# Kernel tuning notes

Hardware: AMD Instinct MI355X
Metric: run time of the kernel (lower is better)

## Reference

```python
import jax, jax.numpy as jnp
import numpy as np
from jax import lax

B, HIST, FC, N, F = 64, 24, 24, 1000, 8
EMB, HID, NEMB, OUT = 32, 64, 1000, 1
IN = EMB + OUT  # GRU input dim


def setup_inputs() -> dict:
    key = jax.random.key(0)
    ks = jax.random.split(key, 11)
    X = jax.random.normal(ks[0], (B, HIST + FC, N, F), jnp.float32)
    idx = jax.random.randint(ks[1], (B, HIST + FC, N), 0, NEMB)
    X = X.at[..., -1].set(idx.astype(jnp.float32))  # last channel = spatial ids
    hn = jax.random.normal(ks[2], (B * N, HID), jnp.float32)
    xn = jax.random.normal(ks[3], (B, N, OUT), jnp.float32)
    s = 0.1
    emb_table = jax.random.normal(ks[4], (NEMB, EMB), jnp.float32) * s
    W_ih = jax.random.normal(ks[5], (3 * HID, IN), jnp.float32) * s
    W_hh = jax.random.normal(ks[6], (3 * HID, HID), jnp.float32) * s
    b_ih = jax.random.normal(ks[7], (3 * HID,), jnp.float32) * s
    b_hh = jax.random.normal(ks[8], (3 * HID,), jnp.float32) * s
    W_out = jax.random.normal(ks[9], (OUT, HID), jnp.float32) * s
    b_out = jax.random.normal(ks[10], (OUT,), jnp.float32) * s
    return {"X": X, "hn": hn, "xn": xn, "emb_table": emb_table,
            "W_ih": W_ih, "W_hh": W_hh, "b_ih": b_ih, "b_hh": b_hh,
            "W_out": W_out, "b_out": b_out}


def reference(X, hn, xn, emb_table, W_ih, W_hh, b_ih, b_hh, W_out, b_out):
    # indices for the forecast steps: [FC, B, N]
    idx_seq = X[:, :FC, :, -1].astype(jnp.int32).transpose(1, 0, 2)

    def step(carry, idx_t):
        h, x_prev = carry                      # h: [B*N, HID], x_prev: [B, N, 1]
        emb = emb_table[idx_t]                 # [B, N, EMB] gather
        x = jnp.concatenate([x_prev, emb], axis=-1).reshape(B * N, IN)
        gi = x @ W_ih.T + b_ih                 # [B*N, 3*HID]
        gh = h @ W_hh.T + b_hh
        i_r, i_z, i_n = jnp.split(gi, 3, axis=-1)
        h_r, h_z, h_n = jnp.split(gh, 3, axis=-1)
        r = jax.nn.sigmoid(i_r + h_r)
        z = jax.nn.sigmoid(i_z + h_z)
        n = jnp.tanh(i_n + r * h_n)
        h_new = (1.0 - z) * n + z * h
        out = h_new.reshape(B, N, HID) @ W_out.T + b_out  # [B, N, 1]
        return (h_new, out), out

    _, preds = lax.scan(step, (hn, xn), idx_seq)  # preds: [FC, B, N, 1]
    return preds.transpose(1, 0, 2, 3)            # [B, FC, N, 1]
```

## Files before the change

kernel.cpp:

```cpp
#include <hip/hip_runtime.h>
#include <math.h>

#define BB   64
#define FC   24
#define NN   1000
#define HID  64
#define EMBD 32
#define TT   48
#define FF   8
#define INSZ 33

#define CPB  32
#define TPB  256
#define AST  72
#define XST  40

#define NL2E (-1.4426950408889634f)
#define TL2E ( 2.8853900817779268f)

typedef __attribute__((ext_vector_type(8))) short bf16x8;
typedef __attribute__((ext_vector_type(4))) float f32x4;

static __device__ __forceinline__ unsigned short f2bf(float f) {
    unsigned u = __builtin_bit_cast(unsigned, f);
    u += 0x7FFFu + ((u >> 16) & 1u);
    return (unsigned short)(u >> 16);
}
static __device__ __forceinline__ unsigned cvt_pk_bf16(float a, float b) {
    unsigned r;
    asm("v_cvt_pk_bf16_f32 %0, %1, %2" : "=v"(r) : "v"(a), "v"(b));
    return r;
}
static __device__ __forceinline__ bf16x8 mk_bf8(float4 lo, float4 hi, float s) {
    union { unsigned u[4]; bf16x8 v; } r;
    r.u[0] = cvt_pk_bf16(lo.x * s, lo.y * s);
    r.u[1] = cvt_pk_bf16(lo.z * s, lo.w * s);
    r.u[2] = cvt_pk_bf16(hi.x * s, hi.y * s);
    r.u[3] = cvt_pk_bf16(hi.z * s, hi.w * s);
    return r.v;
}

static __device__ __forceinline__ void lds_barrier() {
    __builtin_amdgcn_sched_barrier(0);
    asm volatile("s_waitcnt lgkmcnt(0)" ::: "memory");
    __builtin_amdgcn_s_barrier();
    __builtin_amdgcn_sched_barrier(0);
}

__global__ __launch_bounds__(TPB) __attribute__((amdgpu_waves_per_eu(3)))
void gru_decoder(
    const float* __restrict__ X,
    const float* __restrict__ hn0,
    const float* __restrict__ xn,
    const float* __restrict__ emb,
    const float* __restrict__ Wih,
    const float* __restrict__ Whh,
    const float* __restrict__ bih,
    const float* __restrict__ bhh,
    const float* __restrict__ Wout,
    const float* __restrict__ bout,
    float* __restrict__ out)
{
    __shared__ __align__(16) unsigned short Abuf[CPB * AST];
    __shared__ __align__(16) unsigned short Xt[2][CPB * XST];
    __shared__ int   idxbuf[FC * CPB];
    __shared__ float xbuf[CPB];

    const int tid  = threadIdx.x;
    const int lane = tid & 63;
    const int g    = tid >> 6;
    const int quad = lane >> 4;
    const int l15  = lane & 15;
    const int jcol = g * 16 + l15;
    const int rowb = quad * 4;
    const int cell0 = blockIdx.x * CPB;

    for (int e = tid; e < FC * CPB; e += TPB) {
        int t = e >> 5, m = e & 31;
        int cell = cell0 + m;
        int b = cell / NN, n = cell - b * NN;
        idxbuf[t * CPB + m] = (int)X[(((size_t)b * TT + t) * NN + n) * FF + 7];
    }
    if (tid < CPB) xbuf[tid] = xn[cell0 + tid];

    bf16x8 Bf[3][2];
    #pragma unroll
    for (int gate = 0; gate < 3; ++gate) {
        const float s = (gate < 2) ? NL2E : TL2E;
        #pragma unroll
        for (int ks = 0; ks < 2; ++ks) {
            const float* src = Whh + (size_t)(gate * HID + jcol) * HID + ks * 32 + quad * 8;
            Bf[gate][ks] = mk_bf8(*(const float4*)src, *(const float4*)(src + 4), s);
        }
    }
    bf16x8 BX[3];
    #pragma unroll
    for (int gate = 0; gate < 3; ++gate) {
        const float s = (gate < 2) ? NL2E : TL2E;
        const float* src = Wih + (size_t)(gate * HID + jcol) * INSZ + 1 + quad * 8;
        union { unsigned u[4]; bf16x8 v; } f;
        #pragma unroll
        for (int p = 0; p < 4; ++p)
            f.u[p] = cvt_pk_bf16(src[2 * p] * s, src[2 * p + 1] * s);
        BX[gate] = f.v;
    }

    const float w0r2 = NL2E * Wih[(size_t)jcol * INSZ];
    const float w0z2 = NL2E * Wih[(size_t)(HID + jcol) * INSZ];
    const float w0n2 = TL2E * Wih[(size_t)(2 * HID + jcol) * INSZ];
    const float br2  = NL2E * (bih[jcol] + bhh[jcol]);
    const float bz2  = NL2E * (bih[HID + jcol] + bhh[HID + jcol]);
    const float bni2 = TL2E * bih[2 * HID + jcol];
    const float bhn2 = TL2E * bhh[2 * HID + jcol];
    const float bout0 = bout[0];

    float wout4[4];
    #pragma unroll
    for (int e2 = 0; e2 < 4; ++e2) wout4[e2] = Wout[l15 * 4 + e2];
    const int od_c = g * 4 + quad;
    size_t ob[2];
    #pragma unroll
    for (int gx = 0; gx < 2; ++gx) {
        int cell = cell0 + gx * 16 + od_c;
        int b = cell / NN, n = cell - b * NN;
        ob[gx] = (size_t)b * FC * NN + n;
    }

    float hold0[4], hold1[4];
    #pragma unroll
    for (int rr = 0; rr < 4; ++rr) {
        int m0 = rowb + rr, m1 = 16 + rowb + rr;
        float h0 = hn0[((size_t)cell0 + m0) * HID + jcol];
        float h1 = hn0[((size_t)cell0 + m1) * HID + jcol];
        hold0[rr] = h0; hold1[rr] = h1;
        Abuf[m0 * AST + jcol] = f2bf(h0);
        Abuf[m1 * AST + jcol] = f2bf(h1);
    }
    __syncthreads();

    const int r8 = tid >> 3, k4 = (tid & 7) * 4;
    {
        int idx = idxbuf[r8];
        float4 e4 = *(const float4*)(emb + (size_t)idx * EMBD + k4);
        *(uint2*)&Xt[0][r8 * XST + k4] =
            make_uint2(cvt_pk_bf16(e4.x, e4.y), cvt_pk_bf16(e4.z, e4.w));
    }
    __syncthreads();

    auto PHASE_A = [&](int X16, const unsigned short* Xc,
                       f32x4& ar, f32x4& az, f32x4& ani, f32x4& ang) {
        const bf16x8 a0 = *(const bf16x8*)&Abuf[(X16 + l15) * AST + quad * 8];
        const bf16x8 a1 = *(const bf16x8*)&Abuf[(X16 + l15) * AST + 32 + quad * 8];
        const bf16x8 x0 = *(const bf16x8*)&Xc[(X16 + l15) * XST + quad * 8];
        const f32x4 z4 = {0.f, 0.f, 0.f, 0.f};
        ar  = __builtin_amdgcn_mfma_f32_16x16x32_bf16(x0, BX[0], z4, 0, 0, 0);
        ar  = __builtin_amdgcn_mfma_f32_16x16x32_bf16(a0, Bf[0][0], ar, 0, 0, 0);
        ar  = __builtin_amdgcn_mfma_f32_16x16x32_bf16(a1, Bf[0][1], ar, 0, 0, 0);
        az  = __builtin_amdgcn_mfma_f32_16x16x32_bf16(x0, BX[1], z4, 0, 0, 0);
        az  = __builtin_amdgcn_mfma_f32_16x16x32_bf16(a0, Bf[1][0], az, 0, 0, 0);
        az  = __builtin_amdgcn_mfma_f32_16x16x32_bf16(a1, Bf[1][1], az, 0, 0, 0);
        ani = __builtin_amdgcn_mfma_f32_16x16x32_bf16(x0, BX[2], z4, 0, 0, 0);
        ang = __builtin_amdgcn_mfma_f32_16x16x32_bf16(a0, Bf[2][0], z4, 0, 0, 0);
        ang = __builtin_amdgcn_mfma_f32_16x16x32_bf16(a1, Bf[2][1], ang, 0, 0, 0);
    };

    auto PHASE_B = [&](int X16, f32x4& ar, f32x4& az, f32x4& ani, f32x4& ang,
                       float* hold) {
        #pragma unroll
        for (int rp = 0; rp < 2; ++rp) {
            float h2[2];
            #pragma unroll
            for (int k = 0; k < 2; ++k) {
                const int rr = rp * 2 + k;
                const int m  = X16 + rowb + rr;
                const float xp = xbuf[m];
                float sr = fmaf(w0r2, xp, ar[rr] + br2);
                float r  = __builtin_amdgcn_rcpf(1.0f + __builtin_amdgcn_exp2f(sr));
                float sz = fmaf(w0z2, xp, az[rr] + bz2);
                float z  = __builtin_amdgcn_rcpf(1.0f + __builtin_amdgcn_exp2f(sz));
                float v  = fmaf(r, ang[rr] + bhn2, fmaf(w0n2, xp, ani[rr] + bni2));
                float e  = __builtin_amdgcn_exp2f(v);
                float nv = fmaf(-2.0f, __builtin_amdgcn_rcpf(e + 1.0f), 1.0f);
                float hnew = fmaf(z, hold[rr] - nv, nv);
                hold[rr] = hnew;
                h2[k] = hnew;
            }
            unsigned pk = cvt_pk_bf16(h2[0], h2[1]);
            const int m0 = X16 + rowb + rp * 2;
            Abuf[m0 * AST + jcol]       = (unsigned short)pk;
            Abuf[(m0 + 1) * AST + jcol] = (unsigned short)(pk >> 16);
        }
    };

    auto OUTDOT = [&](int gx, int tw, bool wr) {
        const int X16 = gx << 4;
        const uint2 hv = *(const uint2*)&Abuf[(X16 + od_c) * AST + l15 * 4];
        float o;
        o = wout4[0] * __builtin_bit_cast(float, hv.x << 16);
        o = fmaf(wout4[1], __builtin_bit_cast(float, hv.x & 0xFFFF0000u), o);
        o = fmaf(wout4[2], __builtin_bit_cast(float, hv.y << 16), o);
        o = fmaf(wout4[3], __builtin_bit_cast(float, hv.y & 0xFFFF0000u), o);
        o += __shfl_xor(o, 1);
        o += __shfl_xor(o, 2);
        o += __shfl_xor(o, 4);
        o += __shfl_xor(o, 8);
        if (l15 == 0) {
            float oo = o + bout0;
            out[ob[gx] + (size_t)tw * NN] = oo;
            if (wr) xbuf[X16 + od_c] = oo;
        }
    };

    f32x4 ar0, az0, ani0, ang0;
    f32x4 ar1, az1, ani1, ang1;

    #pragma unroll 2
    for (int t = 0; t < FC; ++t) {
        const int tn = (t + 1 < FC) ? t + 1 : FC - 1;
        const int nidx = idxbuf[tn * CPB + r8];
        const float4 e4 = *(const float4*)(emb + (size_t)nidx * EMBD + k4);
        const unsigned short* Xc = Xt[t & 1];

        PHASE_A(0, Xc, ar0, az0, ani0, ang0);
        if (t > 0) {
            PHASE_B(16, ar1, az1, ani1, ang1, hold1);
            OUTDOT(0, t - 1, true);
        }
        lds_barrier();

        PHASE_A(16, Xc, ar1, az1, ani1, ang1);
        PHASE_B(0, ar0, az0, ani0, ang0, hold0);
        if (t > 0) OUTDOT(1, t - 1, true);
        *(uint2*)&Xt[(t + 1) & 1][r8 * XST + k4] =
            make_uint2(cvt_pk_bf16(e4.x, e4.y), cvt_pk_bf16(e4.z, e4.w));
        lds_barrier();
    }

    PHASE_B(16, ar1, az1, ani1, ang1, hold1);
    OUTDOT(0, FC - 1, false);
    lds_barrier();
    OUTDOT(1, FC - 1, false);
}

extern "C" void kernel_launch(void* const* d_in, const int* in_sizes, int n_in,
                              void* d_out, int out_size, void* d_ws, size_t ws_size,
                              hipStream_t stream) {
    (void)in_sizes; (void)n_in; (void)out_size; (void)d_ws; (void)ws_size;
    const float* X    = (const float*)d_in[0];
    const float* hn   = (const float*)d_in[1];
    const float* xn   = (const float*)d_in[2];
    const float* emb  = (const float*)d_in[3];
    const float* Wih  = (const float*)d_in[4];
    const float* Whh  = (const float*)d_in[5];
    const float* bih  = (const float*)d_in[6];
    const float* bhh  = (const float*)d_in[7];
    const float* Wout = (const float*)d_in[8];
    const float* bout = (const float*)d_in[9];
    float* out = (float*)d_out;

    const int blocks = (BB * NN) / CPB;
    gru_decoder<<<blocks, TPB, 0, stream>>>(X, hn, xn, emb, Wih, Whh,
                                            bih, bhh, Wout, bout, out);
}
```

Before: 274.6 us.

## Fold output projection into MFMA and halve cells per block with double-buffered h

Each block now handles 16 cells instead of 32. The output dot product W_out·h is computed as two extra MFMAs every wave redundantly issues on the same h tile, so the shuffle reductions and the xbuf round-trip through shared memory go away. The bout term is folded into the gate biases and x_prev is taken directly from the MFMA accumulator. h is double-buffered in LDS so each step needs only one barrier instead of two, and waves_per_eu rises to 4. The trade-off is twice as many blocks and redundant output MFMAs in every wave. The unshown launch code must also grid over 16-cell blocks.

```diff
diff --git a/kernel.cpp b/kernel.cpp
--- a/kernel.cpp
+++ b/kernel.cpp
@@ -10,7 +10,7 @@
 #define FF   8
 #define INSZ 33
 
-#define CPB  32
+#define CPB  16
 #define TPB  256
 #define AST  72
 #define XST  40
@@ -47,7 +47,7 @@
     __builtin_amdgcn_sched_barrier(0);
 }
 
-__global__ __launch_bounds__(TPB) __attribute__((amdgpu_waves_per_eu(3)))
+__global__ __launch_bounds__(TPB) __attribute__((amdgpu_waves_per_eu(4)))
 void gru_decoder(
     const float* __restrict__ X,
     const float* __restrict__ hn0,
@@ -61,10 +61,10 @@
     const float* __restrict__ bout,
     float* __restrict__ out)
 {
-    __shared__ __align__(16) unsigned short Abuf[CPB * AST];
+    __shared__ __align__(16) unsigned short Hbuf[2][CPB * AST];
     __shared__ __align__(16) unsigned short Xt[2][CPB * XST];
     __shared__ int   idxbuf[FC * CPB];
-    __shared__ float xbuf[CPB];
+    __shared__ float xbuf0[CPB];
 
     const int tid  = threadIdx.x;
     const int lane = tid & 63;
@@ -76,12 +76,12 @@
     const int cell0 = blockIdx.x * CPB;
 
     for (int e = tid; e < FC * CPB; e += TPB) {
-        int t = e >> 5, m = e & 31;
+        int t = e >> 4, m = e & 15;
         int cell = cell0 + m;
         int b = cell / NN, n = cell - b * NN;
         idxbuf[t * CPB + m] = (int)X[(((size_t)b * TT + t) * NN + n) * FF + 7];
     }
-    if (tid < CPB) xbuf[tid] = xn[cell0 + tid];
+    if (tid < CPB) xbuf0[tid] = xn[cell0 + tid];
 
     bf16x8 Bf[3][2];
     #pragma unroll
@@ -104,42 +104,48 @@
             f.u[p] = cvt_pk_bf16(src[2 * p] * s, src[2 * p + 1] * s);
         BX[gate] = f.v;
     }
+    bf16x8 BO[2];
+    #pragma unroll
+    for (int ks = 0; ks < 2; ++ks) {
+        const float* src = Wout + ks * 32 + quad * 8;
+        union { unsigned u[4]; bf16x8 v; } f;
+        #pragma unroll
+        for (int p = 0; p < 4; ++p)
+            f.u[p] = cvt_pk_bf16(src[2 * p], src[2 * p + 1]);
+        BO[ks] = f.v;
+    }
 
     const float w0r2 = NL2E * Wih[(size_t)jcol * INSZ];
     const float w0z2 = NL2E * Wih[(size_t)(HID + jcol) * INSZ];
     const float w0n2 = TL2E * Wih[(size_t)(2 * HID + jcol) * INSZ];
-    const float br2  = NL2E * (bih[jcol] + bhh[jcol]);
-    const float bz2  = NL2E * (bih[HID + jcol] + bhh[HID + jcol]);
-    const float bni2 = TL2E * bih[2 * HID + jcol];
-    const float bhn2 = TL2E * bhh[2 * HID + jcol];
     const float bout0 = bout[0];
-
-    float wout4[4];
-    #pragma unroll
-    for (int e2 = 0; e2 < 4; ++e2) wout4[e2] = Wout[l15 * 4 + e2];
-    const int od_c = g * 4 + quad;
-    size_t ob[2];
-    #pragma unroll
-    for (int gx = 0; gx < 2; ++gx) {
-        int cell = cell0 + gx * 16 + od_c;
+    const float br2p  = NL2E * (bih[jcol] + bhh[jcol]) + w0r2 * bout0;
+    const float bz2p  = NL2E * (bih[HID + jcol] + bhh[HID + jcol]) + w0z2 * bout0;
+    const float bni2p = TL2E * bih[2 * HID + jcol] + w0n2 * bout0;
+    const float bhn2  = TL2E * bhh[2 * HID + jcol];
+
+    size_t sb[4];
+    #pragma unroll
+    for (int rr = 0; rr < 4; ++rr) {
+        int cell = cell0 + rowb + rr;
         int b = cell / NN, n = cell - b * NN;
-        ob[gx] = (size_t)b * FC * NN + n;
-    }
-
-    float hold0[4], hold1[4];
+        sb[rr] = (size_t)b * FC * NN + n;
+    }
+    const bool storer = (g == 0) && (l15 == 0);
+
+    float hold[4];
     #pragma unroll
     for (int rr = 0; rr < 4; ++rr) {
-        int m0 = rowb + rr, m1 = 16 + rowb + rr;
-        float h0 = hn0[((size_t)cell0 + m0) * HID + jcol];
-        float h1 = hn0[((size_t)cell0 + m1) * HID + jcol];
-        hold0[rr] = h0; hold1[rr] = h1;
-        Abuf[m0 * AST + jcol] = f2bf(h0);
-        Abuf[m1 * AST + jcol] = f2bf(h1);
+        int m = rowb + rr;
+        float h = hn0[((size_t)cell0 + m) * HID + jcol];
+        hold[rr] = h;
+        Hbuf[0][m * AST + jcol] = f2bf(h);
     }
     __syncthreads();
 
     const int r8 = tid >> 3, k4 = (tid & 7) * 4;
-    {
+    const bool stg = tid < CPB * 8;
+    if (stg) {
         int idx = idxbuf[r8];
         float4 e4 = *(const float4*)(emb + (size_t)idx * EMBD + k4);
         *(uint2*)&Xt[0][r8 * XST + k4] =
@@ -147,11 +153,12 @@
     }
     __syncthreads();
 
-    auto PHASE_A = [&](int X16, const unsigned short* Xc,
-                       f32x4& ar, f32x4& az, f32x4& ani, f32x4& ang) {
-        const bf16x8 a0 = *(const bf16x8*)&Abuf[(X16 + l15) * AST + quad * 8];
-        const bf16x8 a1 = *(const bf16x8*)&Abuf[(X16 + l15) * AST + 32 + quad * 8];
-        const bf16x8 x0 = *(const bf16x8*)&Xc[(X16 + l15) * XST + quad * 8];
+    f32x4 ar, az, ani, ang, ao;
+
+    auto PHASE_A = [&](const unsigned short* Hb, const unsigned short* Xc) {
+        const bf16x8 a0 = *(const bf16x8*)&Hb[l15 * AST + quad * 8];
+        const bf16x8 a1 = *(const bf16x8*)&Hb[l15 * AST + 32 + quad * 8];
+        const bf16x8 x0 = *(const bf16x8*)&Xc[l15 * XST + quad * 8];
         const f32x4 z4 = {0.f, 0.f, 0.f, 0.f};
         ar  = __builtin_amdgcn_mfma_f32_16x16x32_bf16(x0, BX[0], z4, 0, 0, 0);
         ar  = __builtin_amdgcn_mfma_f32_16x16x32_bf16(a0, Bf[0][0], ar, 0, 0, 0);
@@ -162,84 +169,89 @@
         ani = __builtin_amdgcn_mfma_f32_16x16x32_bf16(x0, BX[2], z4, 0, 0, 0);
         ang = __builtin_amdgcn_mfma_f32_16x16x32_bf16(a0, Bf[2][0], z4, 0, 0, 0);
         ang = __builtin_amdgcn_mfma_f32_16x16x32_bf16(a1, Bf[2][1], ang, 0, 0, 0);
+        ao  = __builtin_amdgcn_mfma_f32_16x16x32_bf16(a0, BO[0], z4, 0, 0, 0);
+        ao  = __builtin_amdgcn_mfma_f32_16x16x32_bf16(a1, BO[1], ao, 0, 0, 0);
     };
 
-    auto PHASE_B = [&](int X16, f32x4& ar, f32x4& az, f32x4& ani, f32x4& ang,
-                       float* hold) {
+    auto GATES = [&](int rr, float xv) -> float {
+        float sr = fmaf(w0r2, xv, ar[rr] + br2p);
+        float r  = __builtin_amdgcn_rcpf(1.0f + __builtin_amdgcn_exp2f(sr));
+        float sz = fmaf(w0z2, xv, az[rr] + bz2p);
+        float z  = __builtin_amdgcn_rcpf(1.0f + __builtin_amdgcn_exp2f(sz));
+        float v  = fmaf(r, ang[rr] + bhn2, fmaf(w0n2, xv, ani[rr] + bni2p));
+        float e  = __builtin_amdgcn_exp2f(v);
+        float nv = fmaf(-2.0f, __builtin_amdgcn_rcpf(e + 1.0f), 1.0f);
+        float hnew = fmaf(z, hold[rr] - nv, nv);
+        hold[rr] = hnew;
+        return hnew;
+    };
+
+    auto WRITE_H = [&](unsigned short* Hw, int rp, float h0, float h1) {
+        unsigned pk = cvt_pk_bf16(h0, h1);
+        const int m0 = rowb + rp * 2;
+        Hw[m0 * AST + jcol]       = (unsigned short)pk;
+        Hw[(m0 + 1) * AST + jcol] = (unsigned short)(pk >> 16);
+    };
+
+    {
+        float4 e4 = {0.f, 0.f, 0.f, 0.f};
+        if (stg) {
+            int idx = idxbuf[1 * CPB + r8];
+            e4 = *(const float4*)(emb + (size_t)idx * EMBD + k4);
+        }
+        PHASE_A(Hbuf[0], Xt[0]);
         #pragma unroll
         for (int rp = 0; rp < 2; ++rp) {
-            float h2[2];
+            float h0 = GATES(rp * 2,     xbuf0[rowb + rp * 2]     - bout0);
+            float h1 = GATES(rp * 2 + 1, xbuf0[rowb + rp * 2 + 1] - bout0);
+            WRITE_H(Hbuf[1], rp, h0, h1);
+        }
+        if (stg)
+            *(uint2*)&Xt[1][r8 * XST + k4] =
+                make_uint2(cvt_pk_bf16(e4.x, e4.y), cvt_pk_bf16(e4.z, e4.w));
+        lds_barrier();
+    }
+
+    #pragma unroll 2
+    for (int t = 1; t < FC; ++t) {
+        const int tn = (t + 1 < FC) ? t + 1 : FC - 1;
+        float4 e4 = {0.f, 0.f, 0.f, 0.f};
+        if (stg)
+            e4 = *(const float4*)(emb + (size_t)idxbuf[tn * CPB + r8] * EMBD + k4);
+
+        PHASE_A(Hbuf[t & 1], Xt[t & 1]);
+
+        unsigned short* Hw = Hbuf[(t + 1) & 1];
+        #pragma unroll
+        for (int rp = 0; rp < 2; ++rp) {
+            float h0 = GATES(rp * 2,     ao[rp * 2]);
+            float h1 = GATES(rp * 2 + 1, ao[rp * 2 + 1]);
+            WRITE_H(Hw, rp, h0, h1);
+        }
+        if (storer) {
             #pragma unroll
-            for (int k = 0; k < 2; ++k) {
-                const int rr = rp * 2 + k;
-                const int m  = X16 + rowb + rr;
-                const float xp = xbuf[m];
-                float sr = fmaf(w0r2, xp, ar[rr] + br2);
-                float r  = __builtin_amdgcn_rcpf(1.0f + __builtin_amdgcn_exp2f(sr));
-                float sz = fmaf(w0z2, xp, az[rr] + bz2);
-                float z  = __builtin_amdgcn_rcpf(1.0f + __builtin_amdgcn_exp2f(sz));
-                float v  = fmaf(r, ang[rr] + bhn2, fmaf(w0n2, xp, ani[rr] + bni2));
-                float e  = __builtin_amdgcn_exp2f(v);
-                float nv = fmaf(-2.0f, __builtin_amdgcn_rcpf(e + 1.0f), 1.0f);
-                float hnew = fmaf(z, hold[rr] - nv, nv);
-                hold[rr] = hnew;
-                h2[k] = hnew;
-            }
-            unsigned pk = cvt_pk_bf16(h2[0], h2[1]);
-            const int m0 = X16 + rowb + rp * 2;
-            Abuf[m0 * AST + jcol]       = (unsigned short)pk;
-            Abuf[(m0 + 1) * AST + jcol] = (unsigned short)(pk >> 16);
-        }
-    };
-
-    auto OUTDOT = [&](int gx, int tw, bool wr) {
-        const int X16 = gx << 4;
-        const uint2 hv = *(const uint2*)&Abuf[(X16 + od_c) * AST + l15 * 4];
-        float o;
-        o = wout4[0] * __builtin_bit_cast(float, hv.x << 16);
-        o = fmaf(wout4[1], __builtin_bit_cast(float, hv.x & 0xFFFF0000u), o);
-        o = fmaf(wout4[2], __builtin_bit_cast(float, hv.y << 16), o);
-        o = fmaf(wout4[3], __builtin_bit_cast(float, hv.y & 0xFFFF0000u), o);
-        o += __shfl_xor(o, 1);
-        o += __shfl_xor(o, 2);
-        o += __shfl_xor(o, 4);
-        o += __shfl_xor(o, 8);
-        if (l15 == 0) {
-            float oo = o + bout0;
-            out[ob[gx] + (size_t)tw * NN] = oo;
-            if (wr) xbuf[X16 + od_c] = oo;
-        }
-    };
-
-    f32x4 ar0, az0, ani0, ang0;
-    f32x4 ar1, az1, ani1, ang1;
-
-    #pragma unroll 2
-    for (int t = 0; t < FC; ++t) {
-        const int tn = (t + 1 < FC) ? t + 1 : FC - 1;
-        const int nidx = idxbuf[tn * CPB + r8];
-        const float4 e4 = *(const float4*)(emb + (size_t)nidx * EMBD + k4);
-        const unsigned short* Xc = Xt[t & 1];
-
-        PHASE_A(0, Xc, ar0, az0, ani0, ang0);
-        if (t > 0) {
-            PHASE_B(16, ar1, az1, ani1, ang1, hold1);
-            OUTDOT(0, t - 1, true);
-        }
+            for (int rr = 0; rr < 4; ++rr)
+                out[sb[rr] + (size_t)(t - 1) * NN] = ao[rr] + bout0;
+        }
+        if (stg)
+            *(uint2*)&Xt[(t + 1) & 1][r8 * XST + k4] =
+                make_uint2(cvt_pk_bf16(e4.x, e4.y), cvt_pk_bf16(e4.z, e4.w));
         lds_barrier();
-
-        PHASE_A(16, Xc, ar1, az1, ani1, ang1);
-        PHASE_B(0, ar0, az0, ani0, ang0, hold0);
-        if (t > 0) OUTDOT(1, t - 1, true);
-        *(uint2*)&Xt[(t + 1) & 1][r8 * XST + k4] =
-            make_uint2(cvt_pk_bf16(e4.x, e4.y), cvt_pk_bf16(e4.z, e4.w));
-        lds_barrier();
-    }
-
-    PHASE_B(16, ar1, az1, ani1, ang1, hold1);
-    OUTDOT(0, FC - 1, false);
-    lds_barrier();
-    OUTDOT(1, FC - 1, false);
+    }
+
+    {
+        const unsigned short* Hb = Hbuf[FC & 1];
+        const bf16x8 a0 = *(const bf16x8*)&Hb[l15 * AST + quad * 8];
+        const bf16x8 a1 = *(const bf16x8*)&Hb[l15 * AST + 32 + quad * 8];
+        const f32x4 z4 = {0.f, 0.f, 0.f, 0.f};
+        f32x4 o = __builtin_amdgcn_mfma_f32_16x16x32_bf16(a0, BO[0], z4, 0, 0, 0);
+        o = __builtin_amdgcn_mfma_f32_16x16x32_bf16(a1, BO[1], o, 0, 0, 0);
+        if (storer) {
+            #pragma unroll
+            for (int rr = 0; rr < 4; ++rr)
+                out[sb[rr] + (size_t)(FC - 1) * NN] = o[rr] + bout0;
+        }
+    }
 }
 
 extern "C" void kernel_launch(void* const* d_in, const int* in_sizes, int n_in,
```

After: 268.8 us. 1.02x faster.
